# Kernel tuning notes

Measured on AMD Instinct MI355X. Metric: run time of the kernel, lower is better.

## Reference

```python
import jax, jax.numpy as jnp
import numpy as np

NU, NI, D, H, E, NQ = 200000, 100000, 64, 64, 1000000, 100000


def setup_inputs() -> dict:
    key = jax.random.key(0)
    ks = jax.random.split(key, 16)
    s = 0.05
    inp = {
        'user_emb': jax.random.normal(ks[0], (NU, D), jnp.float32) * s,
        'item_emb': jax.random.normal(ks[1], (NI, D), jnp.float32) * s,
        'W1': jax.random.normal(ks[2], (6, D, H), jnp.float32) * s,
        'b1': jnp.zeros((6, H), jnp.float32),
        'W2': jax.random.normal(ks[3], (6, H, H), jnp.float32) * s,
        'b2': jnp.zeros((6, H), jnp.float32),
        'dec_w1': jax.random.normal(ks[4], (2 * H, H), jnp.float32) * s,
        'dec_b1': jnp.zeros((H,), jnp.float32),
        'dec_w2': jax.random.normal(ks[5], (H, 4), jnp.float32) * s,
        'dec_b2': jnp.zeros((4,), jnp.float32),
    }
    for name, k in [('edge_view', ks[6]), ('edge_save', ks[7]), ('edge_buy', ks[8])]:
        src = jax.random.randint(k, (E,), 0, NU, jnp.int64 if jax.config.jax_enable_x64 else jnp.int32)
        dst = jax.random.randint(jax.random.fold_in(k, 1), (E,), 0, NI, src.dtype)
        inp[name] = jnp.stack([src, dst])  # [2, E], row0=user, row1=item
    inp['user_ids'] = jax.random.randint(ks[9], (NQ,), 0, NU, jnp.int32)
    inp['item_ids'] = jax.random.randint(ks[10], (NQ,), 0, NI, jnp.int32)
    return inp


def _gcn_conv(h_src, src, dst, n_src, n_dst, W, b):
    # GCNConv (add_self_loops=False) on a bipartite relation:
    # out[d] = sum_e 1/sqrt(deg_src[src_e]) * 1/sqrt(deg_dst[d]) * (x W)[src_e] + b
    h = h_src @ W  # [n_src, H]
    ones = jnp.ones(src.shape[0], h.dtype)
    deg_s = jax.ops.segment_sum(ones, src, num_segments=n_src)
    deg_d = jax.ops.segment_sum(ones, dst, num_segments=n_dst)
    inv_s = jnp.where(deg_s > 0, jax.lax.rsqrt(jnp.maximum(deg_s, 1.0)), 0.0)
    inv_d = jnp.where(deg_d > 0, jax.lax.rsqrt(jnp.maximum(deg_d, 1.0)), 0.0)
    norm = inv_s[src] * inv_d[dst]  # [E]
    msg = h[src] * norm[:, None]    # [E, H]  (dominant memory traffic)
    return jax.ops.segment_sum(msg, dst, num_segments=n_dst) + b


def _hetero_layer(xu, xi, edges, W, b, aggr):
    # relations 0..2: user->item (view,save,buy); 3..5: item->user (reverses)
    item_outs = jnp.stack([_gcn_conv(xu, e[0], e[1], NU, NI, W[k], b[k])
                           for k, e in enumerate(edges)])
    user_outs = jnp.stack([_gcn_conv(xi, e[1], e[0], NI, NU, W[k + 3], b[k + 3])
                           for k, e in enumerate(edges)])
    if aggr == 'max':
        return user_outs.max(0), item_outs.max(0)
    return user_outs.sum(0), item_outs.sum(0)


def reference(user_emb, item_emb, W1, b1, W2, b2, dec_w1, dec_b1, dec_w2, dec_b2,
              edge_view, edge_save, edge_buy, user_ids, item_ids):
    edges = [edge_view, edge_save, edge_buy]
    xu, xi = _hetero_layer(user_emb, item_emb, edges, W1, b1, 'max')
    xu, xi = jax.nn.relu(xu), jax.nn.relu(xi)
    xu, xi = _hetero_layer(xu, xi, edges, W2, b2, 'sum')
    edge_emb = jnp.concatenate([xu[user_ids], xi[item_ids]], axis=-1)  # [NQ, 2H]
    h = jax.nn.relu(edge_emb @ dec_w1 + dec_b1)  # dropout in eval mode = identity
    return h @ dec_w2 + dec_b2  # [NQ, 4]
```

## Files before the change

### kernel.cpp

```cpp
#include <hip/hip_runtime.h>
#include <hip/hip_fp16.h>
#include <math.h>

#define NUV 200000
#define NIV 100000
#define EV  1000000
#define NQV 100000
#define NC  (3 * NIV + 3 * NUV)
#define EV6 (6 * EV)

struct alignas(8) H4 { __half2 a, b; };

__global__ __launch_bounds__(256) void k_tohalf(const float* __restrict__ inu,
                                                const float* __restrict__ ini,
                                                __half* __restrict__ outu,
                                                __half* __restrict__ outi) {
    const int NU4 = NUV * 16;
    const int NTOT = NU4 + NIV * 16;
    int i = blockIdx.x * 256 + threadIdx.x;
    if (i < NTOT) {
        const float* in = (i < NU4) ? inu : ini;
        __half* out = (i < NU4) ? outu : outi;
        int j = (i < NU4) ? i : (i - NU4);
        float4 v = ((const float4*)in)[j];
        H4 o;
        o.a = __floats2half2_rn(v.x, v.y);
        o.b = __floats2half2_rn(v.z, v.w);
        ((H4*)out)[j] = o;
    }
}

__global__ __launch_bounds__(256) void k_count(const int* __restrict__ e0,
                                               const int* __restrict__ e1,
                                               const int* __restrict__ e2,
                                               int* __restrict__ cnt,
                                               int* __restrict__ rk_i,
                                               int* __restrict__ rk_u) {
    int k = blockIdx.y;
    const int* ed = (k == 0) ? e0 : (k == 1) ? e1 : e2;
    int e = blockIdx.x * 256 + threadIdx.x;
    if (e < EV) {
        int u = ed[e], i = ed[EV + e];
        rk_i[(size_t)k * EV + e] = atomicAdd(&cnt[k * NIV + i], 1);
        rk_u[(size_t)k * EV + e] = atomicAdd(&cnt[3 * NIV + k * NUV + u], 1);
    }
}

__global__ __launch_bounds__(256) void k_scan1(const int* __restrict__ cnt,
                                               int* __restrict__ S,
                                               int* __restrict__ bsum,
                                               float* __restrict__ invs) {
    __shared__ int tmp[256];
    int idx = blockIdx.x * 256 + threadIdx.x;
    int v = (idx < NC) ? cnt[idx] : 0;
    if (idx < NC) invs[idx] = (v > 0) ? (1.0f / sqrtf((float)v)) : 0.0f;
    tmp[threadIdx.x] = v;
    __syncthreads();
    for (int off = 1; off < 256; off <<= 1) {
        int t = (threadIdx.x >= off) ? tmp[threadIdx.x - off] : 0;
        __syncthreads();
        tmp[threadIdx.x] += t;
        __syncthreads();
    }
    if (idx < NC) S[idx] = tmp[threadIdx.x] - v;
    if (threadIdx.x == 255) bsum[blockIdx.x] = tmp[255];
}

__global__ __launch_bounds__(64) void k_scan2(int* __restrict__ bsum, int nb) {
    int lane = threadIdx.x;
    int carry = 0;
    for (int base = 0; base < nb; base += 64) {
        int i = base + lane;
        int v = (i < nb) ? bsum[i] : 0;
        int orig = v;
        #pragma unroll
        for (int off = 1; off < 64; off <<= 1) {
            int t = __shfl_up(v, off, 64);
            if (lane >= off) v += t;
        }
        if (i < nb) bsum[i] = carry + v - orig;
        carry += __shfl(v, 63, 64);
    }
}

__global__ __launch_bounds__(256) void k_scan3(int* __restrict__ S,
                                               const int* __restrict__ bsum) {
    int idx = blockIdx.x * 256 + threadIdx.x;
    if (idx < NC) S[idx] += bsum[blockIdx.x];
    if (idx == 0) S[NC] = EV6;
}

__global__ __launch_bounds__(256) void k_fill(const int* __restrict__ e0,
                                              const int* __restrict__ e1,
                                              const int* __restrict__ e2,
                                              const float* __restrict__ invs,
                                              const int* __restrict__ S,
                                              const int* __restrict__ rk_i,
                                              const int* __restrict__ rk_u,
                                              float2* __restrict__ ent) {
    int k = blockIdx.y;
    const int* ed = (k == 0) ? e0 : (k == 1) ? e1 : e2;
    int e = blockIdx.x * 256 + threadIdx.x;
    if (e < EV) {
        int u = ed[e], i = ed[EV + e];
        float nm = invs[k * NIV + i] * invs[3 * NIV + k * NUV + u];
        int p1 = S[k * NIV + i] + rk_i[(size_t)k * EV + e];
        ent[p1] = make_float2(__int_as_float(u), nm);
        int p2 = S[3 * NIV + k * NUV + u] + rk_u[(size_t)k * EV + e];
        ent[p2] = make_float2(__int_as_float(i), nm);
    }
}

template <int MODE, bool HOUT>
__global__ __launch_bounds__(256, 4) void k_agg(const __half* __restrict__ x_i,
                                                const __half* __restrict__ x_u,
                                                const float2* __restrict__ ent,
                                                const int* __restrict__ S,
                                                const float* __restrict__ Wall,
                                                const float* __restrict__ ball,
                                                void* __restrict__ out_i,
                                                void* __restrict__ out_u) {
    __shared__ float sAcc[3][16 * 68];
    const int nb_i = NIV / 16;
    bool item_side = blockIdx.x < nb_i;
    const __half* x = item_side ? x_i : x_u;
    const float* Wb = item_side ? Wall : Wall + 3 * 4096;
    const float* bb = item_side ? ball : ball + 192;
    void* outp      = item_side ? out_i : out_u;
    int n_dst       = item_side ? NIV : NUV;
    int seg_base    = item_side ? 0 : 3 * NIV;
    int d0          = (item_side ? blockIdx.x : (blockIdx.x - nb_i)) * 16;

    int wave = threadIdx.x >> 6;
    int lane = threadIdx.x & 63;
    int eg   = lane >> 4;
    int fq   = lane & 15;
    int r2 = threadIdx.x >> 4;
    int g  = threadIdx.x & 15;

    int sb[3][5];
    #pragma unroll
    for (int k = 0; k < 3; k++) {
        int idx = seg_base + k * n_dst + d0 + wave * 4;
        #pragma unroll
        for (int j = 0; j < 5; j++) sb[k][j] = S[idx + j];
    }
    int mx = 0;
    #pragma unroll
    for (int k = 0; k < 3; k++)
        #pragma unroll
        for (int n = 0; n < 4; n++) mx = max(mx, sb[k][n + 1] - sb[k][n]);
    int maxit = (mx + 3) >> 2;

    float acc[3][4][4];
    #pragma unroll
    for (int k = 0; k < 3; k++)
        #pragma unroll
        for (int n = 0; n < 4; n++)
            #pragma unroll
            for (int j = 0; j < 4; j++) acc[k][n][j] = 0.f;

    for (int it = 0; it < maxit; it++) {
        int base = (it << 2) + eg;
        float2 ev[3][4];
        #pragma unroll
        for (int k = 0; k < 3; k++)
            #pragma unroll
            for (int n = 0; n < 4; n++) {
                int p = sb[k][n] + base;
                int pc = min(p, EV6 - 1);
                ev[k][n] = ent[pc];
            }
        float2 raw[3][4];
        float nm[3][4];
        #pragma unroll
        for (int k = 0; k < 3; k++)
            #pragma unroll
            for (int n = 0; n < 4; n++) {
                int p = sb[k][n] + base;
                nm[k][n] = (p < sb[k][n + 1]) ? ev[k][n].y : 0.f;
                int s = __float_as_int(ev[k][n].x);
                raw[k][n] = *(const float2*)(x + (size_t)s * 64 + fq * 4);
            }
        #pragma unroll
        for (int k = 0; k < 3; k++)
            #pragma unroll
            for (int n = 0; n < 4; n++) {
                const __half2* h2 = (const __half2*)&raw[k][n];
                float2 f0 = __half22float2(h2[0]);
                float2 f1 = __half22float2(h2[1]);
                acc[k][n][0] = fmaf(f0.x, nm[k][n], acc[k][n][0]);
                acc[k][n][1] = fmaf(f0.y, nm[k][n], acc[k][n][1]);
                acc[k][n][2] = fmaf(f1.x, nm[k][n], acc[k][n][2]);
                acc[k][n][3] = fmaf(f1.y, nm[k][n], acc[k][n][3]);
            }
    }
    #pragma unroll
    for (int k = 0; k < 3; k++)
        #pragma unroll
        for (int n = 0; n < 4; n++) {
            #pragma unroll
            for (int j = 0; j < 4; j++) {
                acc[k][n][j] += __shfl_xor(acc[k][n][j], 16, 64);
                acc[k][n][j] += __shfl_xor(acc[k][n][j], 32, 64);
            }
            if (lane < 16)
                *(float4*)&sAcc[k][(wave * 4 + n) * 68 + fq * 4] =
                    make_float4(acc[k][n][0], acc[k][n][1], acc[k][n][2], acc[k][n][3]);
        }
    __syncthreads();

    float4 res = make_float4(0.f, 0.f, 0.f, 0.f);
    #pragma unroll
    for (int k = 0; k < 3; k++) {
        const float* Wk = Wb + (size_t)k * 4096;
        float4 y = *(const float4*)&bb[k * 64 + g * 4];
        #pragma unroll
        for (int c = 0; c < 64; c++) {
            float a = sAcc[k][r2 * 68 + c];
            float4 w = *(const float4*)&Wk[c * 64 + g * 4];
            y.x = fmaf(a, w.x, y.x);
            y.y = fmaf(a, w.y, y.y);
            y.z = fmaf(a, w.z, y.z);
            y.w = fmaf(a, w.w, y.w);
        }
        if (k == 0) {
            res = y;
        } else if (MODE == 0) {
            res.x = fmaxf(res.x, y.x); res.y = fmaxf(res.y, y.y);
            res.z = fmaxf(res.z, y.z); res.w = fmaxf(res.w, y.w);
        } else {
            res.x += y.x; res.y += y.y; res.z += y.z; res.w += y.w;
        }
    }
    if (MODE == 0) {
        res.x = fmaxf(res.x, 0.f); res.y = fmaxf(res.y, 0.f);
        res.z = fmaxf(res.z, 0.f); res.w = fmaxf(res.w, 0.f);
    }
    if (HOUT) {
        H4 o;
        o.a = __floats2half2_rn(res.x, res.y);
        o.b = __floats2half2_rn(res.z, res.w);
        *(H4*)((__half*)outp + (size_t)(d0 + r2) * 64 + g * 4) = o;
    } else {
        *(float4*)((float*)outp + (size_t)(d0 + r2) * 64 + g * 4) = res;
    }
}

__global__ __launch_bounds__(256) void k_decoder(const float* __restrict__ xu,
                                                 const float* __restrict__ xi,
                                                 const int* __restrict__ uids,
                                                 const int* __restrict__ iids,
                                                 const float* __restrict__ w1,
                                                 const float* __restrict__ b1,
                                                 const float* __restrict__ w2,
                                                 const float* __restrict__ b2,
                                                 float* __restrict__ out) {
    __shared__ float sW1[128 * 64];
    __shared__ float sE[16 * 132];
    __shared__ float sH[16 * 68];
    __shared__ float sW2[64 * 4];
    {
        const float4* wsrc = (const float4*)w1;
        float4* wdst = (float4*)sW1;
        #pragma unroll
        for (int i = 0; i < 8; i++) wdst[threadIdx.x + 256 * i] = wsrc[threadIdx.x + 256 * i];
        if (threadIdx.x < 64) {
            float4 v = ((const float4*)w2)[threadIdx.x];
            ((float4*)sW2)[threadIdx.x] = v;
        }
    }
    int q0 = blockIdx.x * 16;
    {
        int q = threadIdx.x >> 4;
        int p = threadIdx.x & 15;
        int uid = uids[q0 + q];
        int iid = iids[q0 + q];
        float4 vu = *(const float4*)&xu[(size_t)uid * 64 + p * 4];
        float4 vi = *(const float4*)&xi[(size_t)iid * 64 + p * 4];
        *(float4*)&sE[q * 132 + p * 4] = vu;
        *(float4*)&sE[q * 132 + 64 + p * 4] = vi;
    }
    __syncthreads();
    {
        int r = threadIdx.x >> 4;
        int g = threadIdx.x & 15;
        float4 y = *(const float4*)&b1[g * 4];
        #pragma unroll
        for (int c = 0; c < 128; c++) {
            float a = sE[r * 132 + c];
            float4 w = *(const float4*)&sW1[c * 64 + g * 4];
            y.x = fmaf(a, w.x, y.x);
            y.y = fmaf(a, w.y, y.y);
            y.z = fmaf(a, w.z, y.z);
            y.w = fmaf(a, w.w, y.w);
        }
        y.x = fmaxf(y.x, 0.f); y.y = fmaxf(y.y, 0.f);
        y.z = fmaxf(y.z, 0.f); y.w = fmaxf(y.w, 0.f);
        *(float4*)&sH[r * 68 + g * 4] = y;
    }
    __syncthreads();
    if (threadIdx.x < 64) {
        int q = threadIdx.x >> 2;
        int oc = threadIdx.x & 3;
        float acc = b2[oc];
        #pragma unroll
        for (int c = 0; c < 64; c++)
            acc = fmaf(sH[q * 68 + c], sW2[c * 4 + oc], acc);
        out[(size_t)(q0 + q) * 4 + oc] = acc;
    }
}

extern "C" void kernel_launch(void* const* d_in, const int* in_sizes, int n_in,
                              void* d_out, int out_size, void* d_ws, size_t ws_size,
                              hipStream_t stream) {
    const float* user_emb = (const float*)d_in[0];
    const float* item_emb = (const float*)d_in[1];
    const float* W1 = (const float*)d_in[2];
    const float* b1 = (const float*)d_in[3];
    const float* W2 = (const float*)d_in[4];
    const float* b2 = (const float*)d_in[5];
    const float* dw1 = (const float*)d_in[6];
    const float* db1 = (const float*)d_in[7];
    const float* dw2 = (const float*)d_in[8];
    const float* db2 = (const float*)d_in[9];
    const int* e0 = (const int*)d_in[10];
    const int* e1 = (const int*)d_in[11];
    const int* e2 = (const int*)d_in[12];
    const int* uids = (const int*)d_in[13];
    const int* iids = (const int*)d_in[14];
    float* out = (float*)d_out;
    (void)in_sizes; (void)n_in; (void)out_size; (void)ws_size;

    char* base = (char*)d_ws;
    size_t off = 0;
    int*    cnt  = (int*)(base + off);    off += (size_t)NC * 4;
    int*    S    = (int*)(base + off);    off += (size_t)(NC + 8) * 4;
    int*    bsum = (int*)(base + off);    off += (size_t)4096 * 4;
    float*  invs = (float*)(base + off);  off += (size_t)NC * 4;
    int*    rki  = (int*)(base + off);    off += (size_t)3 * EV * 4;
    int*    rku  = (int*)(base + off);    off += (size_t)3 * EV * 4;
    float2* ent  = (float2*)(base + off); off += (size_t)EV6 * 8;
    __half* he_u = (__half*)(base + off); off += (size_t)NUV * 64 * 2;
    __half* he_i = (__half*)(base + off); off += (size_t)NIV * 64 * 2;
    __half* xu1h = (__half*)(base + off); off += (size_t)NUV * 64 * 2;
    __half* xi1h = (__half*)(base + off); off += (size_t)NIV * 64 * 2;
    float*  xu2  = (float*)(base + off);  off += (size_t)NUV * 64 * 4;
    float*  xi2  = (float*)(base + off);  off += (size_t)NIV * 64 * 4;

    const int EB  = (EV + 255) / 256;
    const int SB1 = (NC + 255) / 256;
    const int AGGB = NIV / 16 + NUV / 16;
    const int THB = ((NUV + NIV) * 16 + 255) / 256;

    k_tohalf<<<THB, 256, 0, stream>>>(user_emb, item_emb, he_u, he_i);

    hipMemsetAsync(cnt, 0, (size_t)NC * 4, stream);
    k_count<<<dim3(EB, 3), 256, 0, stream>>>(e0, e1, e2, cnt, rki, rku);
    k_scan1<<<SB1, 256, 0, stream>>>(cnt, S, bsum, invs);
    k_scan2<<<1, 64, 0, stream>>>(bsum, SB1);
    k_scan3<<<SB1, 256, 0, stream>>>(S, bsum);
    k_fill<<<dim3(EB, 3), 256, 0, stream>>>(e0, e1, e2, invs, S, rki, rku, ent);

    k_agg<0, true><<<AGGB, 256, 0, stream>>>(he_u, he_i, ent, S, W1, b1, xi1h, xu1h);
    k_agg<1, false><<<AGGB, 256, 0, stream>>>(xu1h, xi1h, ent, S, W2, b2, xi2, xu2);

    k_decoder<<<NQV / 16, 256, 0, stream>>>(xu2, xi2, uids, iids,
                                            dw1, db1, dw2, db2, out);
}
```

Before: 1.651 ms.

## Use per-segment 8-lane subgroups with dynamic task stealing and XCD-aware block remap

Restructures the aggregation kernel so each 8-lane subgroup processes one (relation, node) segment, reading 16-byte half rows and loading only valid edges. Finished subgroups grab the next segment through a shared-memory atomic counter. This replaces the old scheme that padded every wave's 12 segments to the maximum degree. It also remaps block indices so consecutive workgroups land on the same XCD, which should improve L2 locality. The cost is the atomic and shuffle overhead per task, plus fewer gathers in flight per thread.

```diff
diff --git a/kernel.cpp b/kernel.cpp
--- a/kernel.cpp
+++ b/kernel.cpp
@@ -120,96 +120,83 @@
                                                 const float* __restrict__ ball,
                                                 void* __restrict__ out_i,
                                                 void* __restrict__ out_u) {
-    __shared__ float sAcc[3][16 * 68];
+    __shared__ float sAcc[3][16][68];
+    __shared__ int nextT;
+
+    const int NWG = NIV / 16 + NUV / 16;
+    const int q = NWG / 8, r = NWG % 8;
+    int xcd = blockIdx.x % 8, pos = blockIdx.x / 8;
+    int wg = (xcd < r) ? (xcd * (q + 1) + pos) : (r * (q + 1) + (xcd - r) * q + pos);
+
     const int nb_i = NIV / 16;
-    bool item_side = blockIdx.x < nb_i;
+    bool item_side = wg < nb_i;
     const __half* x = item_side ? x_i : x_u;
     const float* Wb = item_side ? Wall : Wall + 3 * 4096;
     const float* bb = item_side ? ball : ball + 192;
     void* outp      = item_side ? out_i : out_u;
     int n_dst       = item_side ? NIV : NUV;
     int seg_base    = item_side ? 0 : 3 * NIV;
-    int d0          = (item_side ? blockIdx.x : (blockIdx.x - nb_i)) * 16;
-
-    int wave = threadIdx.x >> 6;
+    int d0          = (item_side ? wg : (wg - nb_i)) * 16;
+
+    if (threadIdx.x == 0) nextT = 32;
+    __syncthreads();
+
+    int sgid = threadIdx.x >> 3;
+    int ls   = threadIdx.x & 7;
     int lane = threadIdx.x & 63;
-    int eg   = lane >> 4;
-    int fq   = lane & 15;
+
+    int task = sgid;
+    while (task < 48) {
+        int rel = task >> 4, node = task & 15;
+        int idx = seg_base + rel * n_dst + d0 + node;
+        int st = S[idx], en = S[idx + 1];
+
+        float4 a0 = make_float4(0.f, 0.f, 0.f, 0.f);
+        float4 a1 = make_float4(0.f, 0.f, 0.f, 0.f);
+        for (int base = st; base < en; base += 4) {
+            float2 ee[4];
+            #pragma unroll
+            for (int j = 0; j < 4; j++) {
+                float2 e = make_float2(0.0f, 0.0f);
+                if (base + j < en) e = ent[base + j];
+                ee[j] = e;
+            }
+            float4 rr[4];
+            #pragma unroll
+            for (int j = 0; j < 4; j++) {
+                int s = __float_as_int(ee[j].x);
+                rr[j] = *(const float4*)(x + (size_t)s * 64 + ls * 8);
+            }
+            #pragma unroll
+            for (int j = 0; j < 4; j++) {
+                float nm = ee[j].y;
+                const __half2* h2 = (const __half2*)&rr[j];
+                float2 f0 = __half22float2(h2[0]);
+                float2 f1 = __half22float2(h2[1]);
+                float2 f2 = __half22float2(h2[2]);
+                float2 f3 = __half22float2(h2[3]);
+                a0.x = fmaf(f0.x, nm, a0.x);
+                a0.y = fmaf(f0.y, nm, a0.y);
+                a0.z = fmaf(f1.x, nm, a0.z);
+                a0.w = fmaf(f1.y, nm, a0.w);
+                a1.x = fmaf(f2.x, nm, a1.x);
+                a1.y = fmaf(f2.y, nm, a1.y);
+                a1.z = fmaf(f3.x, nm, a1.z);
+                a1.w = fmaf(f3.y, nm, a1.w);
+            }
+        }
+        *(float4*)&sAcc[rel][node][ls * 8]     = a0;
+        *(float4*)&sAcc[rel][node][ls * 8 + 4] = a1;
+
+        int nt = 0;
+        if (ls == 0) nt = atomicAdd(&nextT, 1);
+        nt = __shfl(nt, lane & 56, 64);
+        task = nt;
+    }
+    __syncthreads();
+
     int r2 = threadIdx.x >> 4;
     int g  = threadIdx.x & 15;
-
-    int sb[3][5];
-    #pragma unroll
-    for (int k = 0; k < 3; k++) {
-        int idx = seg_base + k * n_dst + d0 + wave * 4;
-        #pragma unroll
-        for (int j = 0; j < 5; j++) sb[k][j] = S[idx + j];
-    }
-    int mx = 0;
-    #pragma unroll
-    for (int k = 0; k < 3; k++)
-        #pragma unroll
-        for (int n = 0; n < 4; n++) mx = max(mx, sb[k][n + 1] - sb[k][n]);
-    int maxit = (mx + 3) >> 2;
-
-    float acc[3][4][4];
-    #pragma unroll
-    for (int k = 0; k < 3; k++)
-        #pragma unroll
-        for (int n = 0; n < 4; n++)
-            #pragma unroll
-            for (int j = 0; j < 4; j++) acc[k][n][j] = 0.f;
-
-    for (int it = 0; it < maxit; it++) {
-        int base = (it << 2) + eg;
-        float2 ev[3][4];
-        #pragma unroll
-        for (int k = 0; k < 3; k++)
-            #pragma unroll
-            for (int n = 0; n < 4; n++) {
-                int p = sb[k][n] + base;
-                int pc = min(p, EV6 - 1);
-                ev[k][n] = ent[pc];
-            }
-        float2 raw[3][4];
-        float nm[3][4];
-        #pragma unroll
-        for (int k = 0; k < 3; k++)
-            #pragma unroll
-            for (int n = 0; n < 4; n++) {
-                int p = sb[k][n] + base;
-                nm[k][n] = (p < sb[k][n + 1]) ? ev[k][n].y : 0.f;
-                int s = __float_as_int(ev[k][n].x);
-                raw[k][n] = *(const float2*)(x + (size_t)s * 64 + fq * 4);
-            }
-        #pragma unroll
-        for (int k = 0; k < 3; k++)
-            #pragma unroll
-            for (int n = 0; n < 4; n++) {
-                const __half2* h2 = (const __half2*)&raw[k][n];
-                float2 f0 = __half22float2(h2[0]);
-                float2 f1 = __half22float2(h2[1]);
-                acc[k][n][0] = fmaf(f0.x, nm[k][n], acc[k][n][0]);
-                acc[k][n][1] = fmaf(f0.y, nm[k][n], acc[k][n][1]);
-                acc[k][n][2] = fmaf(f1.x, nm[k][n], acc[k][n][2]);
-                acc[k][n][3] = fmaf(f1.y, nm[k][n], acc[k][n][3]);
-            }
-    }
-    #pragma unroll
-    for (int k = 0; k < 3; k++)
-        #pragma unroll
-        for (int n = 0; n < 4; n++) {
-            #pragma unroll
-            for (int j = 0; j < 4; j++) {
-                acc[k][n][j] += __shfl_xor(acc[k][n][j], 16, 64);
-                acc[k][n][j] += __shfl_xor(acc[k][n][j], 32, 64);
-            }
-            if (lane < 16)
-                *(float4*)&sAcc[k][(wave * 4 + n) * 68 + fq * 4] =
-                    make_float4(acc[k][n][0], acc[k][n][1], acc[k][n][2], acc[k][n][3]);
-        }
-    __syncthreads();
-
     float4 res = make_float4(0.f, 0.f, 0.f, 0.f);
     #pragma unroll
     for (int k = 0; k < 3; k++) {
@@ -217,7 +204,7 @@
         float4 y = *(const float4*)&bb[k * 64 + g * 4];
         #pragma unroll
         for (int c = 0; c < 64; c++) {
-            float a = sAcc[k][r2 * 68 + c];
+            float a = sAcc[k][r2][c];
             float4 w = *(const float4*)&Wk[c * 64 + g * 4];
             y.x = fmaf(a, w.x, y.x);
             y.y = fmaf(a, w.y, y.y);
```

Measured after the change: 1.604 ms. -2.8%, faster.
